# Kernel tuning notes

Hardware: AMD Instinct MI355X
Metric: run time of the kernel (lower is better)

The kernel has to match this reference:

```python
import jax, jax.numpy as jnp
import numpy as np

B, S, D, H = 1, 4096, 1024, 16
HD = D // H  # head_dim = 64


def setup_inputs() -> dict:
    key = jax.random.key(0)
    k1, k2, k3 = jax.random.split(key, 3)
    scale = 0.02
    return {
        "x": jax.random.normal(k1, (B, S, D), dtype=jnp.float32),
        "w_qkv": jax.random.normal(k2, (D, 3 * D), dtype=jnp.float32) * scale,
        "b_qkv": jnp.zeros((3 * D,), dtype=jnp.float32),
        "w_proj": jax.random.normal(k3, (D, D), dtype=jnp.float32) * scale,
        "b_proj": jnp.zeros((D,), dtype=jnp.float32),
    }


def reference(x, w_qkv, b_qkv, w_proj, b_proj):
    b, s, d = x.shape
    qkv = x @ w_qkv + b_qkv                      # [b, s, 3d]
    q, k, v = jnp.split(qkv, 3, axis=-1)
    # [b, h, s, hd]
    q = q.reshape(b, s, H, HD).transpose(0, 2, 1, 3)
    k = k.reshape(b, s, H, HD).transpose(0, 2, 1, 3)
    v = v.reshape(b, s, H, HD).transpose(0, 2, 1, 3)
    score = jnp.einsum("bhqd,bhkd->bhqk", q, k) / jnp.sqrt(jnp.float32(HD))
    causal = jnp.tril(jnp.ones((s, s), dtype=bool))
    score = jnp.where(causal, score, -jnp.inf)
    attn = jax.nn.softmax(score, axis=-1)        # dropout omitted (eval mode, p effectively 0)
    out = jnp.einsum("bhqk,bhkd->bhqd", attn, v)  # [b, h, s, hd]
    out = out.transpose(0, 2, 1, 3).reshape(b, s, d)
    return out @ w_proj + b_proj
```

## Files before the change

### kernel.cpp

```cpp
#include <hip/hip_runtime.h>
#include <hip/hip_bf16.h>
#include <math.h>

typedef __bf16 bf16;
typedef __bf16 bf16x8 __attribute__((ext_vector_type(8)));
typedef __bf16 bf16x4 __attribute__((ext_vector_type(4)));
typedef float f32x4 __attribute__((ext_vector_type(4)));
typedef unsigned int u32;
typedef u32 u32x4 __attribute__((ext_vector_type(4)));

#define S_ 4096
#define D_ 1024
#define H_ 16
#define HD_ 64
#define N3_ 3072
#define NSPLIT 4

typedef const __attribute__((address_space(1))) void* gas1_t;
typedef __attribute__((address_space(3))) void* las3_t;
static __device__ __forceinline__ void g2l16(const void* g, void* l) {
  __builtin_amdgcn_global_load_lds((gas1_t)g, (las3_t)l, 16, 0, 0);
}

static __device__ __forceinline__ u32 fbits(float x) {
  union { float f; u32 u; } c; c.f = x; return c.u;
}

__global__ __launch_bounds__(256) void prep_kernel(const float* __restrict__ x,
                                                   bf16* __restrict__ xb,
                                                   const float* __restrict__ w_qkv,
                                                   bf16* __restrict__ wqkvT,
                                                   const float* __restrict__ w_proj,
                                                   bf16* __restrict__ wprojT) {
  __shared__ float t[32][33];
  const int b = blockIdx.x;
  if (b < 4096) {
    int i = (b * 256 + threadIdx.x) * 4;
    float4 v = *(const float4*)(x + i);
    bf16x4 o;
    o.x = (bf16)v.x; o.y = (bf16)v.y; o.z = (bf16)v.z; o.w = (bf16)v.w;
    *(bf16x4*)(xb + i) = o;
    return;
  }
  const float* in; bf16* outp; int ldin, bx, by;
  if (b < 7168) { int b2 = b - 4096; in = w_qkv;  outp = wqkvT;  ldin = N3_; bx = (b2 % 96) * 32; by = (b2 / 96) * 32; }
  else          { int b3 = b - 7168; in = w_proj; outp = wprojT; ldin = D_;  bx = (b3 % 32) * 32; by = (b3 / 32) * 32; }
  const int tx = threadIdx.x & 31, ty = threadIdx.x >> 5;
#pragma unroll
  for (int i = 0; i < 4; ++i)
    t[ty + i * 8][tx] = in[(size_t)(by + ty + i * 8) * ldin + bx + tx];
  __syncthreads();
#pragma unroll
  for (int i = 0; i < 4; ++i)
    outp[(size_t)(bx + ty + i * 8) * D_ + by + tx] = (bf16)t[tx][ty + i * 8];
}

template <int BN>
__global__ __launch_bounds__(256) void gemm_bt(const bf16* __restrict__ A,
                                               const bf16* __restrict__ Bt,
                                               const float* __restrict__ bias,
                                               bf16* __restrict__ outb,
                                               float* __restrict__ outf,
                                               bf16* __restrict__ vTout,
                                               int M, int N, int K,
                                               int qlim, float qscale) {
  constexpr int NT = BN / 32;
  __shared__ bf16 sA[128 * 32];
  __shared__ bf16 sB[BN * 32];
  const int tid = threadIdx.x;
  const int wave = tid >> 6, lane = tid & 63;
  const int col = lane & 15, quad = lane >> 4;
  const int wm = (wave & 1) * 64, wn = (wave >> 1) * (BN / 2);
  const long bm = (long)blockIdx.x * 128, bn = (long)blockIdx.y * BN;
  const int srow = tid >> 2;
  const int soff = (tid & 3) * 8;

  f32x4 acc[4][NT] = {};

  for (int kb = 0; kb < K; kb += 32) {
    __syncthreads();
    g2l16(A + (bm + srow) * (long)K + kb + soff,      &sA[tid * 8]);
    g2l16(A + (bm + 64 + srow) * (long)K + kb + soff, &sA[2048 + tid * 8]);
#pragma unroll
    for (int i = 0; i < BN / 64; ++i)
      g2l16(Bt + (bn + i * 64 + srow) * (long)K + kb + soff, &sB[i * 2048 + tid * 8]);
    __syncthreads();

    bf16x8 af[4], bfr[NT];
#pragma unroll
    for (int t = 0; t < 4; ++t)
      af[t] = *(const bf16x8*)(&sA[(wm + t * 16 + col) * 32 + quad * 8]);
#pragma unroll
    for (int t = 0; t < NT; ++t)
      bfr[t] = *(const bf16x8*)(&sB[(wn + t * 16 + col) * 32 + quad * 8]);
#pragma unroll
    for (int mt = 0; mt < 4; ++mt)
#pragma unroll
      for (int nt = 0; nt < NT; ++nt)
        acc[mt][nt] = __builtin_amdgcn_mfma_f32_16x16x32_bf16(af[mt], bfr[nt], acc[mt][nt], 0, 0, 0);
  }

#pragma unroll
  for (int mt = 0; mt < 4; ++mt) {
#pragma unroll
    for (int nt = 0; nt < NT; ++nt) {
      long gn = bn + wn + nt * 16 + col;
      float bv = bias ? bias[gn] : 0.f;
      if (vTout && gn >= 2 * D_) {
        bf16x4 vv;
        long gm0 = bm + wm + mt * 16 + quad * 4;
#pragma unroll
        for (int i = 0; i < 4; ++i) vv[i] = (bf16)(acc[mt][nt][i] + bv);
        *(bf16x4*)(&vTout[(gn - 2 * D_) * (long)S_ + gm0]) = vv;
      } else {
        float sc = (gn < qlim) ? qscale : 1.0f;
#pragma unroll
        for (int i = 0; i < 4; ++i) {
          long gm = bm + wm + mt * 16 + quad * 4 + i;
          float v = (acc[mt][nt][i] + bv) * sc;
          if (outf) outf[gm * N + gn] = v;
          else      outb[gm * N + gn] = (bf16)v;
        }
      }
    }
  }
}

__device__ __forceinline__ int swz_g(int row) {
  return (row & 3) | ((((row >> 2) ^ (row >> 3)) & 1) << 2);
}

__global__ __launch_bounds__(256) void attn_kernel(const bf16* __restrict__ qkv,
                                                   const bf16* __restrict__ vT,
                                                   bf16* __restrict__ Opart,
                                                   float* __restrict__ lws) {
  __shared__ bf16 sK[2][64 * 64];
  __shared__ bf16 sV[2][64 * 64];
  const int hh = blockIdx.x;
  const int qb = (int)(gridDim.y - 1 - blockIdx.y);
  const int sp = blockIdx.z;
  const int tid = threadIdx.x;
  const int wave = tid >> 6, lane = tid & 63;
  const int col = lane & 15, quad = lane >> 4;
  const int qbase = qb * 128 + wave * 32;

  const bf16* qp0 = qkv + (size_t)(qbase + col) * N3_ + hh * HD_;
  bf16x8 aq[2][2];
  aq[0][0] = *(const bf16x8*)(qp0 + quad * 8);
  aq[0][1] = *(const bf16x8*)(qp0 + 32 + quad * 8);
  aq[1][0] = *(const bf16x8*)(qp0 + 16 * N3_ + quad * 8);
  aq[1][1] = *(const bf16x8*)(qp0 + 16 * N3_ + 32 + quad * 8);

  bf16x8 ones;
#pragma unroll
  for (int j = 0; j < 8; ++j) ones[j] = (bf16)1.0f;

  f32x4 acc[2][4] = {};
  f32x4 acc_l[2] = {};

  const int krow = (col >> 2) * 8 + (col & 3);
  const int niter = 2 * (qb + 1);
  const int base = niter >> 2, rem = niter & 3;
  const int it0 = sp * base + (sp < rem ? sp : rem);
  const int len = base + (sp < rem ? 1 : 0);
  const int it1 = it0 + len;

  int koff[4][2], voff[2][4];
#pragma unroll
  for (int t = 0; t < 4; ++t) {
    int row = (t >> 1) * 32 + (t & 1) * 4 + krow;
    int pc = quad ^ swz_g(row);
    koff[t][0] = row * 64 + pc * 8;
    koff[t][1] = row * 64 + (pc ^ 4) * 8;
  }
#pragma unroll
  for (int c = 0; c < 2; ++c)
#pragma unroll
    for (int n = 0; n < 4; ++n) {
      int row = n * 16 + col;
      voff[c][n] = row * 64 + (((4 * c + quad) ^ swz_g(row)) * 8);
    }

  const int srow = tid >> 2;
  const int sc0 = (tid & 3) * 2;
  const int gs = swz_g(srow);
  const int soff0 = srow * 64 + ((sc0 ^ gs) * 8);
  const int soff1 = srow * 64 + (((sc0 + 1) ^ gs) * 8);

  const bf16* kgp = qkv + D_ + hh * HD_ + (size_t)(it0 * 64 + srow) * N3_ + sc0 * 8;
  const bf16* vgp = vT + (size_t)hh * HD_ * S_ + (size_t)srow * S_ + it0 * 64 + sc0 * 8;

  if (len > 0) {
    *(int4*)(&sK[0][soff0]) = *(const int4*)kgp;
    *(int4*)(&sK[0][soff1]) = *(const int4*)(kgp + 8);
    *(int4*)(&sV[0][soff0]) = *(const int4*)vgp;
    *(int4*)(&sV[0][soff1]) = *(const int4*)(vgp + 8);
    kgp += 64 * N3_;
    vgp += 64;
    __syncthreads();

    for (int j = it0; j < it1; ++j) {
      const int kb = j * 64;
      const int cur = (j - it0) & 1;
      const bool more = (j + 1 < it1);
      int4 pk0, pk1, pv0, pv1;
      if (more) {
        pk0 = *(const int4*)kgp; pk1 = *(const int4*)(kgp + 8);
        pv0 = *(const int4*)vgp; pv1 = *(const int4*)(vgp + 8);
        kgp += 64 * N3_;
        vgp += 64;
      }

      if (kb < qbase + 32) {
        const bool act0 = kb < qbase + 16;
        const bf16* kc = &sK[cur][0];
        const bf16* vc = &sV[cur][0];

        f32x4 st[2][4];
#pragma unroll
        for (int t = 0; t < 4; ++t) {
          bf16x8 bk0 = *(const bf16x8*)(kc + koff[t][0]);
          bf16x8 bk1 = *(const bf16x8*)(kc + koff[t][1]);
          if (act0) {
            f32x4 z = {};
            z = __builtin_amdgcn_mfma_f32_16x16x32_bf16(bk0, aq[0][0], z, 0, 0, 0);
            st[0][t] = __builtin_amdgcn_mfma_f32_16x16x32_bf16(bk1, aq[0][1], z, 0, 0, 0);
          }
          f32x4 z = {};
          z = __builtin_amdgcn_mfma_f32_16x16x32_bf16(bk0, aq[1][0], z, 0, 0, 0);
          st[1][t] = __builtin_amdgcn_mfma_f32_16x16x32_bf16(bk1, aq[1][1], z, 0, 0, 0);
        }

        bf16x8 pfrag[2][2];
#pragma unroll
        for (int s2 = 0; s2 < 2; ++s2) {
          if (s2 == 0 && !act0) continue;
          const int rowbase = qbase + 16 * s2;
          float p[4][4];
          if (kb + 63 <= rowbase) {
#pragma unroll
            for (int t = 0; t < 4; ++t)
#pragma unroll
              for (int r = 0; r < 4; ++r)
                p[t][r] = __builtin_amdgcn_exp2f(st[s2][t][r]);
          } else {
#pragma unroll
            for (int t = 0; t < 4; ++t)
#pragma unroll
              for (int r = 0; r < 4; ++r) {
                int key = kb + (t >> 1) * 32 + quad * 8 + (t & 1) * 4 + r;
                p[t][r] = (key > rowbase + col)
                              ? 0.f
                              : __builtin_amdgcn_exp2f(st[s2][t][r]);
              }
          }
#pragma unroll
          for (int c = 0; c < 2; ++c) {
            union { bf16x8 v; u32x4 u; } pu;
            pu.u[0] = __builtin_amdgcn_perm(fbits(p[2 * c][1]),     fbits(p[2 * c][0]),     0x07060302u);
            pu.u[1] = __builtin_amdgcn_perm(fbits(p[2 * c][3]),     fbits(p[2 * c][2]),     0x07060302u);
            pu.u[2] = __builtin_amdgcn_perm(fbits(p[2 * c + 1][1]), fbits(p[2 * c + 1][0]), 0x07060302u);
            pu.u[3] = __builtin_amdgcn_perm(fbits(p[2 * c + 1][3]), fbits(p[2 * c + 1][2]), 0x07060302u);
            pfrag[s2][c] = pu.v;
          }
        }

#pragma unroll
        for (int c = 0; c < 2; ++c) {
#pragma unroll
          for (int n = 0; n < 4; ++n) {
            bf16x8 bv = *(const bf16x8*)(vc + voff[c][n]);
            if (act0)
              acc[0][n] = __builtin_amdgcn_mfma_f32_16x16x32_bf16(pfrag[0][c], bv, acc[0][n], 0, 0, 0);
            acc[1][n] = __builtin_amdgcn_mfma_f32_16x16x32_bf16(pfrag[1][c], bv, acc[1][n], 0, 0, 0);
          }
          if (act0)
            acc_l[0] = __builtin_amdgcn_mfma_f32_16x16x32_bf16(pfrag[0][c], ones, acc_l[0], 0, 0, 0);
          acc_l[1] = __builtin_amdgcn_mfma_f32_16x16x32_bf16(pfrag[1][c], ones, acc_l[1], 0, 0, 0);
        }
      }

      if (more) {
        bf16* kn = &sK[cur ^ 1][0];
        bf16* vn = &sV[cur ^ 1][0];
        *(int4*)(kn + soff0) = pk0;
        *(int4*)(kn + soff1) = pk1;
        *(int4*)(vn + soff0) = pv0;
        *(int4*)(vn + soff1) = pv1;
      }
      __syncthreads();
    }
  }

  bf16* Op = Opart + (size_t)sp * S_ * D_;
#pragma unroll
  for (int s2 = 0; s2 < 2; ++s2) {
    const int rowbase = qbase + 16 * s2;
    if (col == 0) {
#pragma unroll
      for (int r = 0; r < 4; ++r)
        lws[((size_t)sp * H_ + hh) * S_ + rowbase + quad * 4 + r] = acc_l[s2][r];
    }
#pragma unroll
    for (int n = 0; n < 4; ++n)
#pragma unroll
      for (int r = 0; r < 4; ++r)
        Op[(size_t)(rowbase + quad * 4 + r) * D_ + hh * HD_ + n * 16 + col] =
            (bf16)acc[s2][n][r];
  }
}

__global__ __launch_bounds__(256) void attn_combine(const bf16* __restrict__ Opart,
                                                    const float* __restrict__ lws,
                                                    bf16* __restrict__ outb) {
  int e = (blockIdx.x * 256 + threadIdx.x) * 8;
  int s = e >> 10;
  int h = (e & (D_ - 1)) >> 6;
  float l = 0.f;
#pragma unroll
  for (int sp = 0; sp < NSPLIT; ++sp) l += lws[((size_t)sp * H_ + h) * S_ + s];
  float inv = 1.0f / l;
  float o[8] = {};
#pragma unroll
  for (int sp = 0; sp < NSPLIT; ++sp) {
    bf16x8 a = *(const bf16x8*)(Opart + (size_t)sp * S_ * D_ + e);
#pragma unroll
    for (int j = 0; j < 8; ++j) o[j] += (float)a[j];
  }
  bf16x8 r;
#pragma unroll
  for (int j = 0; j < 8; ++j) r[j] = (bf16)(o[j] * inv);
  *(bf16x8*)(outb + e) = r;
}

extern "C" void kernel_launch(void* const* d_in, const int* in_sizes, int n_in,
                              void* d_out, int out_size, void* d_ws, size_t ws_size,
                              hipStream_t stream) {
  const float* x      = (const float*)d_in[0];
  const float* w_qkv  = (const float*)d_in[1];
  const float* b_qkv  = (const float*)d_in[2];
  const float* w_proj = (const float*)d_in[3];
  const float* b_proj = (const float*)d_in[4];
  float* out = (float*)d_out;

  bf16* xb     = (bf16*)d_ws;
  bf16* wqkvT  = xb + (size_t)S_ * D_;
  bf16* wprojT = wqkvT + (size_t)N3_ * D_;
  bf16* qkv    = wprojT + (size_t)D_ * D_;
  bf16* vT     = qkv + (size_t)S_ * N3_;
  bf16* Opart  = vT + (size_t)D_ * S_;
  float* lws   = (float*)(Opart + (size_t)NSPLIT * S_ * D_);
  bf16* attn   = xb;

  const float QSCALE = 0.125f * 1.44269504088896f;

  prep_kernel<<<dim3(8192), 256, 0, stream>>>(x, xb, w_qkv, wqkvT, w_proj, wprojT);
  gemm_bt<128><<<dim3(S_ / 128, N3_ / 128), 256, 0, stream>>>(
      xb, wqkvT, b_qkv, qkv, nullptr, vT, S_, N3_, D_, D_, QSCALE);
  attn_kernel<<<dim3(H_, S_ / 128, NSPLIT), 256, 0, stream>>>(qkv, vT, Opart, lws);
  attn_combine<<<dim3((S_ * D_) / 2048), 256, 0, stream>>>(Opart, lws, attn);
  gemm_bt<64><<<dim3(S_ / 128, D_ / 64), 256, 0, stream>>>(
      attn, wprojT, b_proj, nullptr, out, nullptr, S_, D_, D_, 0, 1.0f);
}
```

Before: 214.3 us.

## Pre-pack K and V into MFMA fragment order and drop LDS staging in attention

The QKV GEMM epilogue now writes V straight into a per-lane MFMA fragment layout, and a new repackK kernel rearranges K the same way into a spare workspace buffer. The attention kernel then reads K/V fragments directly from global memory with coalesced per-lane 16-byte loads. This removes the shared-memory double buffer, the swizzle math and the per-iteration barriers. The trade-off is an extra kernel launch plus a K round trip through memory, and global-load latency that is no longer hidden by explicit prefetching.

```diff
diff --git a/kernel.cpp b/kernel.cpp
--- a/kernel.cpp
+++ b/kernel.cpp
@@ -61,7 +61,7 @@
                                                const float* __restrict__ bias,
                                                bf16* __restrict__ outb,
                                                float* __restrict__ outf,
-                                               bf16* __restrict__ vTout,
+                                               bf16* __restrict__ vF,
                                                int M, int N, int K,
                                                int qlim, float qscale) {
   constexpr int NT = BN / 32;
@@ -106,12 +106,17 @@
     for (int nt = 0; nt < NT; ++nt) {
       long gn = bn + wn + nt * 16 + col;
       float bv = bias ? bias[gn] : 0.f;
-      if (vTout && gn >= 2 * D_) {
+      if (vF && gn >= 2 * D_) {
+        int hd = (int)gn - 2 * D_;
+        int hh2 = hd >> 6, nn = (hd >> 4) & 3, colp = hd & 15;
+        long key0 = bm + wm + mt * 16 + quad * 4;
+        int kb64 = (int)(key0 >> 6), kl = (int)(key0 & 63);
+        int cc = kl >> 5, qp2 = (kl >> 3) & 3, j0 = kl & 7;
         bf16x4 vv;
-        long gm0 = bm + wm + mt * 16 + quad * 4;
 #pragma unroll
         for (int i = 0; i < 4; ++i) vv[i] = (bf16)(acc[mt][nt][i] + bv);
-        *(bf16x4*)(&vTout[(gn - 2 * D_) * (long)S_ + gm0]) = vv;
+        *(bf16x4*)(&vF[((((size_t)(hh2 * 64 + kb64) * 2 + cc) * 4 + nn) * 64 +
+                        qp2 * 16 + colp) * 8 + j0]) = vv;
       } else {
         float sc = (gn < qlim) ? qscale : 1.0f;
 #pragma unroll
@@ -126,16 +131,29 @@
   }
 }
 
-__device__ __forceinline__ int swz_g(int row) {
-  return (row & 3) | ((((row >> 2) ^ (row >> 3)) & 1) << 2);
+__global__ __launch_bounds__(256) void repackK(const bf16* __restrict__ qkv,
+                                               bf16* __restrict__ kF) {
+  __shared__ bf16 sK[64 * 72];
+  const int hh = blockIdx.x, kb64 = blockIdx.y;
+  const int tid = threadIdx.x;
+  const int srow = tid >> 2, sc = (tid & 3) * 16;
+  const bf16* src = qkv + (size_t)(kb64 * 64 + srow) * N3_ + D_ + hh * HD_ + sc;
+  *(int4*)(&sK[srow * 72 + sc])     = *(const int4*)src;
+  *(int4*)(&sK[srow * 72 + sc + 8]) = *(const int4*)(src + 8);
+  __syncthreads();
+  const int lane = tid & 63, col = lane & 15, quad = lane >> 4;
+  const int t = tid >> 6;
+  const int row = (t >> 1) * 32 + (t & 1) * 4 + (col >> 2) * 8 + (col & 3);
+  bf16* dst = kF + ((size_t)(hh * 64 + kb64) * 8 + t * 2) * 512 + lane * 8;
+  *(bf16x8*)(dst)       = *(const bf16x8*)(&sK[row * 72 + quad * 8]);
+  *(bf16x8*)(dst + 512) = *(const bf16x8*)(&sK[row * 72 + 32 + quad * 8]);
 }
 
 __global__ __launch_bounds__(256) void attn_kernel(const bf16* __restrict__ qkv,
-                                                   const bf16* __restrict__ vT,
+                                                   const bf16* __restrict__ kF,
+                                                   const bf16* __restrict__ vF,
                                                    bf16* __restrict__ Opart,
                                                    float* __restrict__ lws) {
-  __shared__ bf16 sK[2][64 * 64];
-  __shared__ bf16 sV[2][64 * 64];
   const int hh = blockIdx.x;
   const int qb = (int)(gridDim.y - 1 - blockIdx.y);
   const int sp = blockIdx.z;
@@ -158,137 +176,81 @@
   f32x4 acc[2][4] = {};
   f32x4 acc_l[2] = {};
 
-  const int krow = (col >> 2) * 8 + (col & 3);
   const int niter = 2 * (qb + 1);
-  const int base = niter >> 2, rem = niter & 3;
-  const int it0 = sp * base + (sp < rem ? sp : rem);
-  const int len = base + (sp < rem ? 1 : 0);
+  const int bse = niter >> 2, rem = niter & 3;
+  const int it0 = sp * bse + (sp < rem ? sp : rem);
+  const int len = bse + (sp < rem ? 1 : 0);
   const int it1 = it0 + len;
 
-  int koff[4][2], voff[2][4];
-#pragma unroll
-  for (int t = 0; t < 4; ++t) {
-    int row = (t >> 1) * 32 + (t & 1) * 4 + krow;
-    int pc = quad ^ swz_g(row);
-    koff[t][0] = row * 64 + pc * 8;
-    koff[t][1] = row * 64 + (pc ^ 4) * 8;
-  }
-#pragma unroll
-  for (int c = 0; c < 2; ++c)
-#pragma unroll
-    for (int n = 0; n < 4; ++n) {
-      int row = n * 16 + col;
-      voff[c][n] = row * 64 + (((4 * c + quad) ^ swz_g(row)) * 8);
-    }
-
-  const int srow = tid >> 2;
-  const int sc0 = (tid & 3) * 2;
-  const int gs = swz_g(srow);
-  const int soff0 = srow * 64 + ((sc0 ^ gs) * 8);
-  const int soff1 = srow * 64 + (((sc0 + 1) ^ gs) * 8);
-
-  const bf16* kgp = qkv + D_ + hh * HD_ + (size_t)(it0 * 64 + srow) * N3_ + sc0 * 8;
-  const bf16* vgp = vT + (size_t)hh * HD_ * S_ + (size_t)srow * S_ + it0 * 64 + sc0 * 8;
-
-  if (len > 0) {
-    *(int4*)(&sK[0][soff0]) = *(const int4*)kgp;
-    *(int4*)(&sK[0][soff1]) = *(const int4*)(kgp + 8);
-    *(int4*)(&sV[0][soff0]) = *(const int4*)vgp;
-    *(int4*)(&sV[0][soff1]) = *(const int4*)(vgp + 8);
-    kgp += 64 * N3_;
-    vgp += 64;
-    __syncthreads();
-
-    for (int j = it0; j < it1; ++j) {
-      const int kb = j * 64;
-      const int cur = (j - it0) & 1;
-      const bool more = (j + 1 < it1);
-      int4 pk0, pk1, pv0, pv1;
-      if (more) {
-        pk0 = *(const int4*)kgp; pk1 = *(const int4*)(kgp + 8);
-        pv0 = *(const int4*)vgp; pv1 = *(const int4*)(vgp + 8);
-        kgp += 64 * N3_;
-        vgp += 64;
-      }
-
-      if (kb < qbase + 32) {
-        const bool act0 = kb < qbase + 16;
-        const bf16* kc = &sK[cur][0];
-        const bf16* vc = &sV[cur][0];
-
-        f32x4 st[2][4];
-#pragma unroll
-        for (int t = 0; t < 4; ++t) {
-          bf16x8 bk0 = *(const bf16x8*)(kc + koff[t][0]);
-          bf16x8 bk1 = *(const bf16x8*)(kc + koff[t][1]);
-          if (act0) {
-            f32x4 z = {};
-            z = __builtin_amdgcn_mfma_f32_16x16x32_bf16(bk0, aq[0][0], z, 0, 0, 0);
-            st[0][t] = __builtin_amdgcn_mfma_f32_16x16x32_bf16(bk1, aq[0][1], z, 0, 0, 0);
+  const bf16* kfp = kF + (size_t)(hh * 64 + it0) * 4096 + lane * 8;
+  const bf16* vfp = vF + (size_t)(hh * 64 + it0) * 4096 + lane * 8;
+
+  for (int j = it0; j < it1; ++j, kfp += 4096, vfp += 4096) {
+    const int kb = j * 64;
+    if (kb >= qbase + 32) break;
+    const bool act0 = kb < qbase + 16;
+
+    f32x4 st[2][4];
+#pragma unroll
+    for (int t = 0; t < 4; ++t) {
+      bf16x8 bk0 = *(const bf16x8*)(kfp + (t * 2) * 512);
+      bf16x8 bk1 = *(const bf16x8*)(kfp + (t * 2 + 1) * 512);
+      if (act0) {
+        f32x4 z = {};
+        z = __builtin_amdgcn_mfma_f32_16x16x32_bf16(bk0, aq[0][0], z, 0, 0, 0);
+        st[0][t] = __builtin_amdgcn_mfma_f32_16x16x32_bf16(bk1, aq[0][1], z, 0, 0, 0);
+      }
+      f32x4 z = {};
+      z = __builtin_amdgcn_mfma_f32_16x16x32_bf16(bk0, aq[1][0], z, 0, 0, 0);
+      st[1][t] = __builtin_amdgcn_mfma_f32_16x16x32_bf16(bk1, aq[1][1], z, 0, 0, 0);
+    }
+
+    bf16x8 pfrag[2][2];
+#pragma unroll
+    for (int s2 = 0; s2 < 2; ++s2) {
+      if (s2 == 0 && !act0) continue;
+      const int rowbase = qbase + 16 * s2;
+      float p[4][4];
+      if (kb + 63 <= rowbase) {
+#pragma unroll
+        for (int t = 0; t < 4; ++t)
+#pragma unroll
+          for (int r = 0; r < 4; ++r)
+            p[t][r] = __builtin_amdgcn_exp2f(st[s2][t][r]);
+      } else {
+#pragma unroll
+        for (int t = 0; t < 4; ++t)
+#pragma unroll
+          for (int r = 0; r < 4; ++r) {
+            int key = kb + (t >> 1) * 32 + quad * 8 + (t & 1) * 4 + r;
+            p[t][r] = (key > rowbase + col)
+                          ? 0.f
+                          : __builtin_amdgcn_exp2f(st[s2][t][r]);
           }
-          f32x4 z = {};
-          z = __builtin_amdgcn_mfma_f32_16x16x32_bf16(bk0, aq[1][0], z, 0, 0, 0);
-          st[1][t] = __builtin_amdgcn_mfma_f32_16x16x32_bf16(bk1, aq[1][1], z, 0, 0, 0);
-        }
-
-        bf16x8 pfrag[2][2];
-#pragma unroll
-        for (int s2 = 0; s2 < 2; ++s2) {
-          if (s2 == 0 && !act0) continue;
-          const int rowbase = qbase + 16 * s2;
-          float p[4][4];
-          if (kb + 63 <= rowbase) {
-#pragma unroll
-            for (int t = 0; t < 4; ++t)
-#pragma unroll
-              for (int r = 0; r < 4; ++r)
-                p[t][r] = __builtin_amdgcn_exp2f(st[s2][t][r]);
-          } else {
-#pragma unroll
-            for (int t = 0; t < 4; ++t)
-#pragma unroll
-              for (int r = 0; r < 4; ++r) {
-                int key = kb + (t >> 1) * 32 + quad * 8 + (t & 1) * 4 + r;
-                p[t][r] = (key > rowbase + col)
-                              ? 0.f
-                              : __builtin_amdgcn_exp2f(st[s2][t][r]);
-              }
-          }
-#pragma unroll
-          for (int c = 0; c < 2; ++c) {
-            union { bf16x8 v; u32x4 u; } pu;
-            pu.u[0] = __builtin_amdgcn_perm(fbits(p[2 * c][1]),     fbits(p[2 * c][0]),     0x07060302u);
-            pu.u[1] = __builtin_amdgcn_perm(fbits(p[2 * c][3]),     fbits(p[2 * c][2]),     0x07060302u);
-            pu.u[2] = __builtin_amdgcn_perm(fbits(p[2 * c + 1][1]), fbits(p[2 * c + 1][0]), 0x07060302u);
-            pu.u[3] = __builtin_amdgcn_perm(fbits(p[2 * c + 1][3]), fbits(p[2 * c + 1][2]), 0x07060302u);
-            pfrag[s2][c] = pu.v;
-          }
-        }
-
-#pragma unroll
-        for (int c = 0; c < 2; ++c) {
-#pragma unroll
-          for (int n = 0; n < 4; ++n) {
-            bf16x8 bv = *(const bf16x8*)(vc + voff[c][n]);
-            if (act0)
-              acc[0][n] = __builtin_amdgcn_mfma_f32_16x16x32_bf16(pfrag[0][c], bv, acc[0][n], 0, 0, 0);
-            acc[1][n] = __builtin_amdgcn_mfma_f32_16x16x32_bf16(pfrag[1][c], bv, acc[1][n], 0, 0, 0);
-          }
-          if (act0)
-            acc_l[0] = __builtin_amdgcn_mfma_f32_16x16x32_bf16(pfrag[0][c], ones, acc_l[0], 0, 0, 0);
-          acc_l[1] = __builtin_amdgcn_mfma_f32_16x16x32_bf16(pfrag[1][c], ones, acc_l[1], 0, 0, 0);
-        }
-      }
-
-      if (more) {
-        bf16* kn = &sK[cur ^ 1][0];
-        bf16* vn = &sV[cur ^ 1][0];
-        *(int4*)(kn + soff0) = pk0;
-        *(int4*)(kn + soff1) = pk1;
-        *(int4*)(vn + soff0) = pv0;
-        *(int4*)(vn + soff1) = pv1;
-      }
-      __syncthreads();
+      }
+#pragma unroll
+      for (int c = 0; c < 2; ++c) {
+        union { bf16x8 v; u32x4 u; } pu;
+        pu.u[0] = __builtin_amdgcn_perm(fbits(p[2 * c][1]),     fbits(p[2 * c][0]),     0x07060302u);
+        pu.u[1] = __builtin_amdgcn_perm(fbits(p[2 * c][3]),     fbits(p[2 * c][2]),     0x07060302u);
+        pu.u[2] = __builtin_amdgcn_perm(fbits(p[2 * c + 1][1]), fbits(p[2 * c + 1][0]), 0x07060302u);
+        pu.u[3] = __builtin_amdgcn_perm(fbits(p[2 * c + 1][3]), fbits(p[2 * c + 1][2]), 0x07060302u);
+        pfrag[s2][c] = pu.v;
+      }
+    }
+
+#pragma unroll
+    for (int c = 0; c < 2; ++c) {
+#pragma unroll
+      for (int n = 0; n < 4; ++n) {
+        bf16x8 bv = *(const bf16x8*)(vfp + (c * 4 + n) * 512);
+        if (act0)
+          acc[0][n] = __builtin_amdgcn_mfma_f32_16x16x32_bf16(pfrag[0][c], bv, acc[0][n], 0, 0, 0);
+        acc[1][n] = __builtin_amdgcn_mfma_f32_16x16x32_bf16(pfrag[1][c], bv, acc[1][n], 0, 0, 0);
+      }
+      if (act0)
+        acc_l[0] = __builtin_amdgcn_mfma_f32_16x16x32_bf16(pfrag[0][c], ones, acc_l[0], 0, 0, 0);
+      acc_l[1] = __builtin_amdgcn_mfma_f32_16x16x32_bf16(pfrag[1][c], ones, acc_l[1], 0, 0, 0);
     }
   }
 
@@ -347,17 +309,19 @@
   bf16* wqkvT  = xb + (size_t)S_ * D_;
   bf16* wprojT = wqkvT + (size_t)N3_ * D_;
   bf16* qkv    = wprojT + (size_t)D_ * D_;
-  bf16* vT     = qkv + (size_t)S_ * N3_;
-  bf16* Opart  = vT + (size_t)D_ * S_;
+  bf16* vF     = qkv + (size_t)S_ * N3_;
+  bf16* Opart  = vF + (size_t)D_ * S_;
   float* lws   = (float*)(Opart + (size_t)NSPLIT * S_ * D_);
+  bf16* kF     = xb;
   bf16* attn   = xb;
 
   const float QSCALE = 0.125f * 1.44269504088896f;
 
   prep_kernel<<<dim3(8192), 256, 0, stream>>>(x, xb, w_qkv, wqkvT, w_proj, wprojT);
   gemm_bt<128><<<dim3(S_ / 128, N3_ / 128), 256, 0, stream>>>(
-      xb, wqkvT, b_qkv, qkv, nullptr, vT, S_, N3_, D_, D_, QSCALE);
-  attn_kernel<<<dim3(H_, S_ / 128, NSPLIT), 256, 0, stream>>>(qkv, vT, Opart, lws);
+      xb, wqkvT, b_qkv, qkv, nullptr, vF, S_, N3_, D_, D_, QSCALE);
+  repackK<<<dim3(H_, S_ / 64), 256, 0, stream>>>(qkv, kF);
+  attn_kernel<<<dim3(H_, S_ / 128, NSPLIT), 256, 0, stream>>>(qkv, kF, vF, Opart, lws);
   attn_combine<<<dim3((S_ * D_) / 2048), 256, 0, stream>>>(Opart, lws, attn);
   gemm_bt<64><<<dim3(S_ / 128, D_ / 64), 256, 0, stream>>>(
       attn, wprojT, b_proj, nullptr, out, nullptr, S_, D_, D_, 0, 1.0f);
```

After: 217.1 us. Within noise of the previous version (+1.3%).
